# Optimization experiments

Hardware: AMD Instinct MI355X
Metric: run time of the kernel (lower is better)

## Reference

```python
import jax, jax.numpy as jnp
import numpy as np

T, S, W, D, C, K = 16, 16, 10, 512, 64, 512  # tasks, shots, ways, z_dim, n_concept, triplets/group


def setup_inputs() -> dict:
    key = jax.random.key(0)
    ks = jax.random.split(key, 12)
    sc = 0.02
    inp = {
        "input_data": jax.random.normal(ks[0], (T, S, W, D), dtype=jnp.float32),
        "triplet_idx": jax.random.randint(ks[1], (T, W, 3, K), 0, S * W, dtype=jnp.int64),
        # proj_inner: Linear(3D -> 2D), ReLU, Linear(2D -> D)
        "W1": jax.random.normal(ks[2], (3 * D, 2 * D), dtype=jnp.float32) * sc,
        "b1": jnp.zeros((2 * D,), dtype=jnp.float32),
        "W2": jax.random.normal(ks[3], (2 * D, D), dtype=jnp.float32) * sc,
        "b2": jnp.zeros((D,), dtype=jnp.float32),
        # proj_outer: Linear(D -> 2D), ReLU, Linear(2D -> D)
        "W3": jax.random.normal(ks[4], (D, 2 * D), dtype=jnp.float32) * sc,
        "b3": jnp.zeros((2 * D,), dtype=jnp.float32),
        "W4": jax.random.normal(ks[5], (2 * D, D), dtype=jnp.float32) * sc,
        "b4": jnp.zeros((D,), dtype=jnp.float32),
        # cls: Linear(D -> C)
        "Wc": jax.random.normal(ks[6], (D, C), dtype=jnp.float32) * sc,
        "bc": jnp.zeros((C,), dtype=jnp.float32),
    }
    return inp


def reference(input_data, triplet_idx, W1, b1, W2, b2, W3, b3, W4, b4, Wc, bc):
    t, s, w, d = input_data.shape
    x = input_data.reshape(t, s * w, d)                     # [T, N, D], N = shot*way
    # gather triplet embeddings: [T, W, 3, K, D]
    emb = x[jnp.arange(t)[:, None, None, None], triplet_idx]
    # permute([1,0,2]).reshape(-1, 3*dim): [T, W, K, 3*D]
    trip = jnp.swapaxes(emb, 2, 3).reshape(t, w, -1, 3 * d)
    # proj_inner MLP then sum over triplets
    h = jax.nn.relu(trip @ W1 + b1) @ W2 + b2               # [T, W, K, D]
    g = jnp.sum(h, axis=2)                                  # [T, W, D]
    # proj_outer MLP -> cls -> softmax
    o = jax.nn.relu(g @ W3 + b3) @ W4 + b4                  # [T, W, D]
    score = o @ Wc + bc                                     # [T, W, C]
    return jax.nn.softmax(score, axis=-1)
```

## Files before the change

### kernel.cpp

```cpp
#include <hip/hip_runtime.h>
#include <hip/hip_bf16.h>

#define T_  16
#define W_  10
#define D_  512
#define SW_ 160
#define N1_ 1024
#define KT_ 512

typedef __bf16 bf16x8 __attribute__((ext_vector_type(8)));
typedef _Float16 f16x8 __attribute__((ext_vector_type(8)));
typedef _Float16 h2v  __attribute__((ext_vector_type(2)));
typedef float  f32x4  __attribute__((ext_vector_type(4)));

__device__ __forceinline__ void async16(const void* g, void* l) {
  __builtin_amdgcn_global_load_lds(
      (__attribute__((address_space(1))) void*)(g),
      (__attribute__((address_space(3))) void*)(l), 16, 0, 0);
}

__device__ __forceinline__ h2v bc2(unsigned u) { return __builtin_bit_cast(h2v, u); }
__device__ __forceinline__ h2v relu2(h2v a) {
  h2v r;
  asm("v_pk_max_f16 %0, %1, 0" : "=v"(r) : "v"(a));
  return r;
}

__global__ __launch_bounds__(256) void prep_all(
    const float* __restrict__ x_in, const float* __restrict__ W1,
    const float* __restrict__ W2, const float* __restrict__ W3,
    const float* __restrict__ W4, const float* __restrict__ Wc,
    const float* __restrict__ b2, const float* __restrict__ b3,
    const float* __restrict__ b4, const float* __restrict__ bc,
    __hip_bfloat16* __restrict__ xbf, __hip_bfloat16* __restrict__ w1t,
    _Float16* __restrict__ w2b, _Float16* __restrict__ w3t,
    _Float16* __restrict__ w4b, _Float16* __restrict__ wct,
    float* __restrict__ b23, float* __restrict__ bc4)
{
  __shared__ float tile[32 * 33];
  const int b = blockIdx.x, tid = threadIdx.x;

  auto cast4h = [&](const float* src, _Float16* dst, int base) {
    int i = (base + tid) << 2;
    float4 v = *(const float4*)(src + i);
    __align__(8) _Float16 o4[4] = {(_Float16)v.x, (_Float16)v.y,
                                   (_Float16)v.z, (_Float16)v.w};
    *(uint2*)(dst + i) = *(const uint2*)o4;
  };
  auto tr32h = [&](const float* src, _Float16* dst, int R, int C, int rt, int ct) {
    int r0 = rt << 5, c0 = ct << 5;
    int c = tid & 31, rr = tid >> 5;
#pragma unroll
    for (int i = 0; i < 4; ++i) {
      int r = rr + i * 8;
      tile[r * 33 + c] = src[(size_t)(r0 + r) * C + c0 + c];
    }
    __syncthreads();
#pragma unroll
    for (int i = 0; i < 4; ++i) {
      int r = rr + i * 8;
      dst[(size_t)(c0 + r) * R + r0 + c] = (_Float16)tile[c * 33 + r];
    }
  };

  if (b < 1280) {
    int i = (b * 256 + tid) << 2;
    float4 v = *(const float4*)(x_in + i);
    __align__(8) __hip_bfloat16 o4[4];
    o4[0] = __float2bfloat16(v.x); o4[1] = __float2bfloat16(v.y);
    o4[2] = __float2bfloat16(v.z); o4[3] = __float2bfloat16(v.w);
    *(uint2*)(xbf + i) = *(const uint2*)o4;
  } else if (b < 2816) {
    int q = b - 1280;
    int r0 = (q >> 5) << 5, c0 = (q & 31) << 5;
    int c = tid & 31, rr = tid >> 5;
#pragma unroll
    for (int i = 0; i < 4; ++i) {
      int r = rr + i * 8;
      tile[r * 33 + c] = W1[(size_t)(r0 + r) * 1024 + c0 + c];
    }
    __syncthreads();
#pragma unroll
    for (int i = 0; i < 4; ++i) {
      int r = rr + i * 8;
      w1t[(size_t)(c0 + r) * 1536 + r0 + c] = __float2bfloat16(tile[c * 33 + r]);
    }
  } else if (b < 3328) {
    cast4h(W2, w2b, (b - 2816) * 256);
  } else if (b < 3840) {
    int q = b - 3328; tr32h(W3, w3t, 512, 1024, q >> 5, q & 31);
  } else if (b < 4352) {
    cast4h(W4, w4b, (b - 3840) * 256);
  } else if (b < 4384) {
    int q = b - 4352; tr32h(Wc, wct, 512, 64, q >> 1, q & 1);
  } else if (b < 4388) {
    int c = (b - 4384) * 256 + tid;
    float s = 0.f;
#pragma unroll 32
    for (int j = 0; j < 512; ++j) s += b2[j] * W3[(size_t)j * 1024 + c];
    b23[c] = 512.f * s + b3[c];
  } else {
    if (tid < 64) {
      float s = 0.f;
#pragma unroll 32
      for (int j = 0; j < 512; ++j) s += b4[j] * Wc[(size_t)j * 64 + tid];
      bc4[tid] = s + bc[tid];
    }
  }
}

__global__ __launch_bounds__(256) void pgemm_wgemm(
    const __hip_bfloat16* __restrict__ xbf,
    const __hip_bfloat16* __restrict__ w1t,
    const float* __restrict__ b1,
    char* __restrict__ pbuf,
    const _Float16* __restrict__ w3t,
    const _Float16* __restrict__ w2b,
    const _Float16* __restrict__ wct,
    const _Float16* __restrict__ w4b,
    _Float16* __restrict__ w23t,
    _Float16* __restrict__ w4ct)
{
  __shared__ __align__(16) char smem[34560];
  const int bx = blockIdx.x;
  const int tid = threadIdx.x;
  const int ln = tid & 63, wv = tid >> 6;
  const int col16 = ln & 15, quad = ln >> 4;

  if (bx >= 512) {
    const int b = bx - 512;
    const _Float16 *A, *Bt;
    _Float16* out;
    int m0, n0;
    if (b < 256) { A = w3t; Bt = w2b; out = w23t; m0 = (b >> 4) << 6; n0 = (b & 15) << 6; }
    else         { A = wct; Bt = w4b; out = w4ct; m0 = 0;             n0 = (b - 256) << 6; }
    char* Abuf = smem;
    char* Bbuf = smem + 16384;

    f32x4 acc[4];
#pragma unroll
    for (int a = 0; a < 4; ++a) acc[a] = (f32x4){0.f, 0.f, 0.f, 0.f};

#pragma unroll 1
    for (int kk = 0; kk < 512; kk += 128) {
      __syncthreads();
#pragma unroll
      for (int p = 0; p < 4; ++p) {
        int i = p * 256 + tid, r = i >> 4, q = i & 15;
        async16(A + (size_t)(m0 + r) * 512 + kk + ((q ^ (r & 7)) << 3), Abuf + (i << 4));
      }
#pragma unroll
      for (int p = 0; p < 4; ++p) {
        int i = p * 256 + tid, r = i >> 4, q = i & 15;
        async16(Bt + (size_t)(n0 + r) * 512 + kk + ((q ^ (r & 7)) << 3), Bbuf + (i << 4));
      }
      __syncthreads();

#pragma unroll
      for (int ks = 0; ks < 4; ++ks) {
        const int qq = (ks << 2) + quad;
        const int rn = (wv << 4) + col16;
        f16x8 bfm = *(const f16x8*)(Bbuf + rn * 256 + ((qq ^ (rn & 7)) << 4));
#pragma unroll
        for (int a = 0; a < 4; ++a) {
          int rm = (a << 4) + col16;
          f16x8 af = *(const f16x8*)(Abuf + rm * 256 + ((qq ^ (rm & 7)) << 4));
          acc[a] = __builtin_amdgcn_mfma_f32_16x16x32_f16(af, bfm, acc[a], 0, 0, 0);
        }
      }
    }

    const int n = n0 + (wv << 4) + col16;
#pragma unroll
    for (int a = 0; a < 4; ++a)
#pragma unroll
      for (int r = 0; r < 4; ++r) {
        size_t row = m0 + (a << 4) + (quad << 2) + r;
        out[row * 1024 + n] = (_Float16)acc[a][r];
      }
    return;
  }

  char* Abuf  = smem;
  char* Bbuf  = smem + 20480;
  char* Ptile = smem;

  const int t   = bx >> 5;
  const int nt  = bx & 31;
  const int n0  = nt << 5;

  const int wr = wv >> 1, wc = wv & 1;

  const __hip_bfloat16* xt = xbf + (size_t)t * (SW_ * D_);

  int aoff[5], lofA[5];
#pragma unroll
  for (int s = 0; s < 5; ++s) {
    int i = s * 256 + tid, r = i >> 3, q = i & 7;
    aoff[s] = r * 512 + ((q ^ (r & 7)) << 3);
    lofA[s] = i << 4;
  }
  int boff[3], lofB[3];
#pragma unroll
  for (int s = 0; s < 3; ++s) {
    int i = s * 256 + tid, r = i >> 3, q = i & 7;
    int nc = r & 31, j = r >> 5;
    boff[s] = (n0 + nc) * 1536 + j * 512 + ((q ^ (r & 7)) << 3);
    lofB[s] = i << 4;
  }

  f32x4 acc[5][3];
#pragma unroll
  for (int a = 0; a < 5; ++a)
#pragma unroll
    for (int b = 0; b < 3; ++b)
      acc[a][b] = (f32x4){0.f, 0.f, 0.f, 0.f};

#pragma unroll 1
  for (int kk = 0; kk < 512; kk += 64) {
    __syncthreads();
#pragma unroll
    for (int s = 0; s < 5; ++s) async16(xt + aoff[s] + kk, Abuf + lofA[s]);
#pragma unroll
    for (int s = 0; s < 3; ++s) async16(w1t + boff[s] + kk, Bbuf + lofB[s]);
    __syncthreads();

#pragma unroll
    for (int ks = 0; ks < 2; ++ks) {
      const int qq = (ks << 2) + quad;
      bf16x8 af[5], bfr[3];
#pragma unroll
      for (int a = 0; a < 5; ++a) {
        int rm = wr * 80 + a * 16 + col16;
        af[a] = *(const bf16x8*)(Abuf + rm * 128 + ((qq ^ (rm & 7)) << 4));
      }
#pragma unroll
      for (int b = 0; b < 3; ++b) {
        int rn = wc * 48 + b * 16 + col16;
        bfr[b] = *(const bf16x8*)(Bbuf + rn * 128 + ((qq ^ (rn & 7)) << 4));
      }
#pragma unroll
      for (int a = 0; a < 5; ++a)
#pragma unroll
        for (int b = 0; b < 3; ++b)
          acc[a][b] = __builtin_amdgcn_mfma_f32_16x16x32_bf16(af[a], bfr[b], acc[a][b], 0, 0, 0);
    }
  }

  __syncthreads();

#pragma unroll
  for (int b = 0; b < 3; ++b) {
    int c = wc * 48 + b * 16 + col16;
    int j = c >> 5, nc = c & 31;
    float bv = (j == 2) ? b1[n0 + nc] : 0.f;
#pragma unroll
    for (int a = 0; a < 5; ++a) {
      int mb = wr * 80 + a * 16 + quad * 4;
#pragma unroll
      for (int r = 0; r < 4; ++r)
        *(_Float16*)(Ptile + (j * 160 + mb + r) * 72 + nc * 2) =
            (_Float16)(acc[a][b][r] + bv);
    }
  }
  __syncthreads();

  char* gP = pbuf + (size_t)bx * 34560;
#pragma unroll
  for (int p = 0; p < 9; ++p) {
    int i = p * 256 + tid;
    if (i < 2160)
      *(uint4*)(gP + (size_t)i * 16) = *(const uint4*)(Ptile + i * 16);
  }
}

__global__ __launch_bounds__(256) void gather_kernel(
    const char* __restrict__ pbuf,
    const int* __restrict__ tidx,
    _Float16* __restrict__ Hsb)
{
  __shared__ __align__(16) char P[34560];
  __shared__ int idx[2][1536];
  __shared__ float red[2][128];
  const int tid = threadIdx.x;
  const int wp  = blockIdx.x;
  const int win = blockIdx.y;
  const int t   = blockIdx.z;
  const int ln = tid & 63, wv = tid >> 6;

  const char* ps = pbuf + (size_t)(t * 32 + win) * 34560;
#pragma unroll
  for (int p = 0; p < 9; ++p) {
    int i = p * 256 + tid;
    if (i < 2160) async16(ps + (size_t)i * 16, P + i * 16);
  }

  const int* isrc = tidx + (size_t)(t * 10 + wp * 2) * 1536;
#pragma unroll
  for (int v = 0; v < 2; ++v) {
    const int* s = isrc + v * 1536;
    int4 ra = *(const int4*)(s + (tid << 2));
    *(int4*)(&idx[v][tid << 2]) =
        make_int4(ra.x * 72, ra.y * 72, ra.z * 72, ra.w * 72);
    if (tid < 128) {
      int4 rb = *(const int4*)(s + 1024 + (tid << 2));
      *(int4*)(&idx[v][1024 + (tid << 2)]) =
          make_int4(rb.x * 72, rb.y * 72, rb.z * 72, rb.w * 72);
    }
  }
  __syncthreads();

  const int nq = tid & 7;
  const int kq = tid >> 3;
  const char* Pt0 = P + (nq << 3);
  const char* Pt1 = Pt0 + 11520;
  const char* Pt2 = Pt0 + 23040;

#pragma unroll
  for (int v = 0; v < 2; ++v) {
    const int* cid = idx[v];
    h2v acc01 = (h2v)0, acc23 = (h2v)0;
#pragma unroll
    for (int u = 0; u < 4; ++u) {
      const int kb = (kq << 4) + (u << 2);
      int4 i0 = *(const int4*)(cid + kb);
      int4 i1 = *(const int4*)(cid + 512 + kb);
      int4 i2 = *(const int4*)(cid + 1024 + kb);
#define STEP(IA, IB, IC)                                                  \
      {                                                                   \
        uint2 p0 = *(const uint2*)(Pt0 + (IA));                           \
        uint2 p1 = *(const uint2*)(Pt1 + (IB));                           \
        uint2 p2 = *(const uint2*)(Pt2 + (IC));                           \
        h2v sx = bc2(p0.x) + bc2(p1.x) + bc2(p2.x);                       \
        h2v sy = bc2(p0.y) + bc2(p1.y) + bc2(p2.y);                       \
        acc01 += relu2(sx);                                               \
        acc23 += relu2(sy);                                               \
      }
      STEP(i0.x, i1.x, i2.x)
      STEP(i0.y, i1.y, i2.y)
      STEP(i0.z, i1.z, i2.z)
      STEP(i0.w, i1.w, i2.w)
#undef STEP
    }

    f32x4 a4 = (f32x4){(float)acc01.x, (float)acc01.y,
                       (float)acc23.x, (float)acc23.y};
#pragma unroll
    for (int off = 8; off <= 32; off <<= 1) {
      a4.x += __shfl_xor(a4.x, off);
      a4.y += __shfl_xor(a4.y, off);
      a4.z += __shfl_xor(a4.z, off);
      a4.w += __shfl_xor(a4.w, off);
    }
    if ((ln >> 3) == 0)
      *(f32x4*)(&red[v][wv * 32 + (nq << 2)]) = a4;
  }
  __syncthreads();
  if (tid < 64) {
    int v = tid >> 5, c = tid & 31;
    float s = red[v][c] + red[v][32 + c] + red[v][64 + c] + red[v][96 + c];
    Hsb[(size_t)(t * 10 + wp * 2 + v) * N1_ + (win << 5) + c] = (_Float16)s;
  }
}

__global__ __launch_bounds__(256) void mid_gemm(
    const _Float16* __restrict__ A,
    const _Float16* __restrict__ Bt,
    const float* __restrict__ bias,
    _Float16* __restrict__ out)
{
  __shared__ __align__(16) char Abuf[40960];
  __shared__ __align__(16) char Bbuf[32768];
  const int tid = threadIdx.x;
  const int n0 = blockIdx.x << 6;
  const int m0 = blockIdx.y * 80;
  const int ln = tid & 63, wv = tid >> 6;
  const int col16 = ln & 15, quad = ln >> 4;

  f32x4 acc[5];
#pragma unroll
  for (int a = 0; a < 5; ++a) acc[a] = (f32x4){0.f, 0.f, 0.f, 0.f};

#pragma unroll 1
  for (int kk = 0; kk < 1024; kk += 256) {
    __syncthreads();
#pragma unroll
    for (int p = 0; p < 10; ++p) {
      int i = p * 256 + tid, r = i >> 5, q = i & 31;
      async16(A + (size_t)(m0 + r) * 1024 + kk + ((q ^ (r & 7)) << 3), Abuf + (i << 4));
    }
#pragma unroll
    for (int p = 0; p < 8; ++p) {
      int i = p * 256 + tid, r = i >> 5, q = i & 31;
      async16(Bt + (size_t)(n0 + r) * 1024 + kk + ((q ^ (r & 7)) << 3), Bbuf + (i << 4));
    }
    __syncthreads();

#pragma unroll
    for (int ks = 0; ks < 8; ++ks) {
      const int qq = (ks << 2) + quad;
      const int rn = (wv << 4) + col16;
      f16x8 bfm = *(const f16x8*)(Bbuf + rn * 512 + ((qq ^ (rn & 7)) << 4));
#pragma unroll
      for (int a = 0; a < 5; ++a) {
        int rm = (a << 4) + col16;
        f16x8 af = *(const f16x8*)(Abuf + rm * 512 + ((qq ^ (rm & 7)) << 4));
        acc[a] = __builtin_amdgcn_mfma_f32_16x16x32_f16(af, bfm, acc[a], 0, 0, 0);
      }
    }
  }

  const int n = n0 + (wv << 4) + col16;
  const float bb = bias[n];
#pragma unroll
  for (int a = 0; a < 5; ++a)
#pragma unroll
    for (int r = 0; r < 4; ++r) {
      float v = fmaxf(acc[a][r] + bb, 0.f);
      out[(size_t)(m0 + (a << 4) + (quad << 2) + r) * 1024 + n] = (_Float16)v;
    }
}

__global__ __launch_bounds__(256) void head_gemm2(
    const _Float16* __restrict__ A,
    const _Float16* __restrict__ Bt,
    const float* __restrict__ bc4,
    float* __restrict__ out)
{
  __shared__ __align__(16) char Abuf[40960];
  __shared__ __align__(16) char Bbuf[32768];
  __shared__ float sc[80 * 64];
  __shared__ float rs[80];
  const int tid = threadIdx.x;
  const int m0 = blockIdx.x * 80;
  const int ln = tid & 63, wv = tid >> 6;
  const int col16 = ln & 15, quad = ln >> 4;

  f32x4 acc[5];
#pragma unroll
  for (int a = 0; a < 5; ++a) acc[a] = (f32x4){0.f, 0.f, 0.f, 0.f};

#pragma unroll 1
  for (int kk = 0; kk < 1024; kk += 256) {
    __syncthreads();
#pragma unroll
    for (int p = 0; p < 10; ++p) {
      int i = p * 256 + tid, r = i >> 5, q = i & 31;
      async16(A + (size_t)(m0 + r) * 1024 + kk + ((q ^ (r & 7)) << 3), Abuf + (i << 4));
    }
#pragma unroll
    for (int p = 0; p < 8; ++p) {
      int i = p * 256 + tid, r = i >> 5, q = i & 31;
      async16(Bt + (size_t)r * 1024 + kk + ((q ^ (r & 7)) << 3), Bbuf + (i << 4));
    }
    __syncthreads();

#pragma unroll
    for (int ks = 0; ks < 8; ++ks) {
      const int qq = (ks << 2) + quad;
      const int rn = (wv << 4) + col16;
      f16x8 bfm = *(const f16x8*)(Bbuf + rn * 512 + ((qq ^ (rn & 7)) << 4));
#pragma unroll
      for (int a = 0; a < 5; ++a) {
        int rm = (a << 4) + col16;
        f16x8 af = *(const f16x8*)(Abuf + rm * 512 + ((qq ^ (rm & 7)) << 4));
        acc[a] = __builtin_amdgcn_mfma_f32_16x16x32_f16(af, bfm, acc[a], 0, 0, 0);
      }
    }
  }

  const int n = (wv << 4) + col16;
  const float bb = bc4[n];
#pragma unroll
  for (int a = 0; a < 5; ++a)
#pragma unroll
    for (int r = 0; r < 4; ++r)
      sc[((a << 4) + (quad << 2) + r) * 64 + n] = acc[a][r] + bb;
  __syncthreads();

  if (tid < 80) {
    float m = -1e30f;
    for (int c = 0; c < 64; ++c) m = fmaxf(m, sc[tid * 64 + c]);
    float s = 0.f;
    for (int c = 0; c < 64; ++c) {
      float e = expf(sc[tid * 64 + c] - m);
      sc[tid * 64 + c] = e;
      s += e;
    }
    rs[tid] = 1.f / s;
  }
  __syncthreads();
#pragma unroll
  for (int p = 0; p < 20; ++p) {
    int f = p * 256 + tid, r = f >> 6, c = f & 63;
    out[(size_t)(m0 + r) * 64 + c] = sc[f] * rs[r];
  }
}

extern "C" void kernel_launch(void* const* d_in, const int* in_sizes, int n_in,
                              void* d_out, int out_size, void* d_ws, size_t ws_size,
                              hipStream_t stream) {
  const float* x_in = (const float*)d_in[0];
  const int*   tidx = (const int*)d_in[1];
  const float* W1 = (const float*)d_in[2];
  const float* b1 = (const float*)d_in[3];
  const float* W2 = (const float*)d_in[4];
  const float* b2 = (const float*)d_in[5];
  const float* W3 = (const float*)d_in[6];
  const float* b3 = (const float*)d_in[7];
  const float* W4 = (const float*)d_in[8];
  const float* b4 = (const float*)d_in[9];
  const float* Wc = (const float*)d_in[10];
  const float* bc = (const float*)d_in[11];
  float* out = (float*)d_out;
  (void)in_sizes; (void)n_in; (void)out_size; (void)ws_size;

  char* ws = (char*)d_ws;
  __hip_bfloat16* xbf  = (__hip_bfloat16*)(ws + 0);
  __hip_bfloat16* w1t  = (__hip_bfloat16*)(ws + 2621440);
  _Float16*       w2b  = (_Float16*)      (ws + 5767168);
  _Float16*       w3t  = (_Float16*)      (ws + 6815744);
  _Float16*       w4b  = (_Float16*)      (ws + 7864320);
  _Float16*       wct  = (_Float16*)      (ws + 8912896);
  float*          b23  = (float*)         (ws + 8978432);
  float*          bc4  = (float*)         (ws + 8982528);
  _Float16*       Hsb  = (_Float16*)      (ws + 8982784);
  _Float16*       w23t = (_Float16*)      (ws + 9310464);
  _Float16*       w4ct = (_Float16*)      (ws + 11407616);
  char*           pbuf = ws + 11538688;
  _Float16*       ub   = (_Float16*)      (ws + 11538688);

  prep_all<<<4389, 256, 0, stream>>>(x_in, W1, W2, W3, W4, Wc, b2, b3, b4, bc,
                                     xbf, w1t, w2b, w3t, w4b, wct, b23, bc4);

  pgemm_wgemm<<<784, 256, 0, stream>>>(xbf, w1t, b1, pbuf,
                                       w3t, w2b, wct, w4b, w23t, w4ct);

  gather_kernel<<<dim3(5, 32, 16), 256, 0, stream>>>(pbuf, tidx, Hsb);

  mid_gemm<<<dim3(16, 2), 256, 0, stream>>>(Hsb, w23t, b23, ub);

  head_gemm2<<<2, 256, 0, stream>>>(ub, w4ct, bc4, out);
}
```

Measured before the change: 160.7 us.

## Fuse triplet gather into projection GEMM and fold head GEMM into mid GEMM

The gather/sum stage now runs inside the projection GEMM block. Each block keeps its projected tile in shared memory and loops over the five way-pairs, double-buffering the triplet indices, so the intermediate buffer is never written to and re-read from global memory. The head GEMM is fused into the mid GEMM epilogue as per-column-block partial scores, and a small softmax kernel sums the partials. The projection K-step also widens from 64 to 128, which enlarges shared memory to 64KB and may reduce occupancy.

```diff
diff --git a/kernel.cpp b/kernel.cpp
--- a/kernel.cpp
+++ b/kernel.cpp
@@ -109,11 +109,12 @@
   }
 }
 
-__global__ __launch_bounds__(256) void pgemm_wgemm(
+__global__ __launch_bounds__(256) void group_wgemm(
     const __hip_bfloat16* __restrict__ xbf,
     const __hip_bfloat16* __restrict__ w1t,
+    const int* __restrict__ tidx,
     const float* __restrict__ b1,
-    char* __restrict__ pbuf,
+    _Float16* __restrict__ Hsb,
     const _Float16* __restrict__ w3t,
     const _Float16* __restrict__ w2b,
     const _Float16* __restrict__ wct,
@@ -121,7 +122,7 @@
     _Float16* __restrict__ w23t,
     _Float16* __restrict__ w4ct)
 {
-  __shared__ __align__(16) char smem[34560];
+  __shared__ __align__(16) char smem[65536];
   const int bx = blockIdx.x;
   const int tid = threadIdx.x;
   const int ln = tid & 63, wv = tid >> 6;
@@ -182,8 +183,10 @@
   }
 
   char* Abuf  = smem;
-  char* Bbuf  = smem + 20480;
+  char* Bbuf  = smem + 40960;
   char* Ptile = smem;
+  int*  ibuf  = (int*)(smem + 34560);
+  float* red  = (float*)(smem + 59136);
 
   const int t   = bx >> 5;
   const int nt  = bx & 31;
@@ -193,17 +196,17 @@
 
   const __hip_bfloat16* xt = xbf + (size_t)t * (SW_ * D_);
 
-  int aoff[5], lofA[5];
-#pragma unroll
-  for (int s = 0; s < 5; ++s) {
-    int i = s * 256 + tid, r = i >> 3, q = i & 7;
+  int aoff[10], lofA[10];
+#pragma unroll
+  for (int s = 0; s < 10; ++s) {
+    int i = s * 256 + tid, r = i >> 4, q = i & 15;
     aoff[s] = r * 512 + ((q ^ (r & 7)) << 3);
     lofA[s] = i << 4;
   }
-  int boff[3], lofB[3];
-#pragma unroll
-  for (int s = 0; s < 3; ++s) {
-    int i = s * 256 + tid, r = i >> 3, q = i & 7;
+  int boff[6], lofB[6];
+#pragma unroll
+  for (int s = 0; s < 6; ++s) {
+    int i = s * 256 + tid, r = i >> 4, q = i & 15;
     int nc = r & 31, j = r >> 5;
     boff[s] = (n0 + nc) * 1536 + j * 512 + ((q ^ (r & 7)) << 3);
     lofB[s] = i << 4;
@@ -217,27 +220,27 @@
       acc[a][b] = (f32x4){0.f, 0.f, 0.f, 0.f};
 
 #pragma unroll 1
-  for (int kk = 0; kk < 512; kk += 64) {
-    __syncthreads();
-#pragma unroll
-    for (int s = 0; s < 5; ++s) async16(xt + aoff[s] + kk, Abuf + lofA[s]);
-#pragma unroll
-    for (int s = 0; s < 3; ++s) async16(w1t + boff[s] + kk, Bbuf + lofB[s]);
-    __syncthreads();
-
-#pragma unroll
-    for (int ks = 0; ks < 2; ++ks) {
+  for (int kk = 0; kk < 512; kk += 128) {
+    __syncthreads();
+#pragma unroll
+    for (int s = 0; s < 10; ++s) async16(xt + aoff[s] + kk, Abuf + lofA[s]);
+#pragma unroll
+    for (int s = 0; s < 6; ++s) async16(w1t + boff[s] + kk, Bbuf + lofB[s]);
+    __syncthreads();
+
+#pragma unroll
+    for (int ks = 0; ks < 4; ++ks) {
       const int qq = (ks << 2) + quad;
       bf16x8 af[5], bfr[3];
 #pragma unroll
       for (int a = 0; a < 5; ++a) {
         int rm = wr * 80 + a * 16 + col16;
-        af[a] = *(const bf16x8*)(Abuf + rm * 128 + ((qq ^ (rm & 7)) << 4));
+        af[a] = *(const bf16x8*)(Abuf + rm * 256 + ((qq ^ (rm & 7)) << 4));
       }
 #pragma unroll
       for (int b = 0; b < 3; ++b) {
         int rn = wc * 48 + b * 16 + col16;
-        bfr[b] = *(const bf16x8*)(Bbuf + rn * 128 + ((qq ^ (rn & 7)) << 4));
+        bfr[b] = *(const bf16x8*)(Bbuf + rn * 256 + ((qq ^ (rn & 7)) << 4));
       }
 #pragma unroll
       for (int a = 0; a < 5; ++a)
@@ -263,120 +266,127 @@
             (_Float16)(acc[a][b][r] + bv);
     }
   }
-  __syncthreads();
-
-  char* gP = pbuf + (size_t)bx * 34560;
-#pragma unroll
-  for (int p = 0; p < 9; ++p) {
-    int i = p * 256 + tid;
-    if (i < 2160)
-      *(uint4*)(gP + (size_t)i * 16) = *(const uint4*)(Ptile + i * 16);
-  }
-}
-
-__global__ __launch_bounds__(256) void gather_kernel(
-    const char* __restrict__ pbuf,
-    const int* __restrict__ tidx,
-    _Float16* __restrict__ Hsb)
-{
-  __shared__ __align__(16) char P[34560];
-  __shared__ int idx[2][1536];
-  __shared__ float red[2][128];
-  const int tid = threadIdx.x;
-  const int wp  = blockIdx.x;
-  const int win = blockIdx.y;
-  const int t   = blockIdx.z;
-  const int ln = tid & 63, wv = tid >> 6;
-
-  const char* ps = pbuf + (size_t)(t * 32 + win) * 34560;
-#pragma unroll
-  for (int p = 0; p < 9; ++p) {
-    int i = p * 256 + tid;
-    if (i < 2160) async16(ps + (size_t)i * 16, P + i * 16);
-  }
-
-  const int* isrc = tidx + (size_t)(t * 10 + wp * 2) * 1536;
-#pragma unroll
-  for (int v = 0; v < 2; ++v) {
-    const int* s = isrc + v * 1536;
-    int4 ra = *(const int4*)(s + (tid << 2));
-    *(int4*)(&idx[v][tid << 2]) =
-        make_int4(ra.x * 72, ra.y * 72, ra.z * 72, ra.w * 72);
-    if (tid < 128) {
-      int4 rb = *(const int4*)(s + 1024 + (tid << 2));
-      *(int4*)(&idx[v][1024 + (tid << 2)]) =
-          make_int4(rb.x * 72, rb.y * 72, rb.z * 72, rb.w * 72);
-    }
-  }
-  __syncthreads();
 
   const int nq = tid & 7;
   const int kq = tid >> 3;
-  const char* Pt0 = P + (nq << 3);
+  const char* Pt0 = Ptile + (nq << 3);
   const char* Pt1 = Pt0 + 11520;
   const char* Pt2 = Pt0 + 23040;
 
+  const int* tsrc = tidx + (size_t)t * 10 * 1536;
+  int4 ra[2], rb[2];
+  auto sst2 = [&](int* dstbase) {
+#pragma unroll
+    for (int v = 0; v < 2; ++v) {
+      int* dst = dstbase + v * 1536;
+      *(int4*)(dst + (tid << 2)) =
+          make_int4(ra[v].x * 72, ra[v].y * 72, ra[v].z * 72, ra[v].w * 72);
+      if (tid < 128)
+        *(int4*)(dst + 1024 + (tid << 2)) =
+            make_int4(rb[v].x * 72, rb[v].y * 72, rb[v].z * 72, rb[v].w * 72);
+    }
+  };
+
 #pragma unroll
   for (int v = 0; v < 2; ++v) {
-    const int* cid = idx[v];
-    h2v acc01 = (h2v)0, acc23 = (h2v)0;
-#pragma unroll
-    for (int u = 0; u < 4; ++u) {
-      const int kb = (kq << 4) + (u << 2);
-      int4 i0 = *(const int4*)(cid + kb);
-      int4 i1 = *(const int4*)(cid + 512 + kb);
-      int4 i2 = *(const int4*)(cid + 1024 + kb);
+    const int* s0 = tsrc + v * 1536;
+    ra[v] = *(const int4*)(s0 + (tid << 2));
+    if (tid < 128) rb[v] = *(const int4*)(s0 + 1024 + (tid << 2));
+  }
+  sst2(ibuf);
+  int cur = 0;
+
+#pragma unroll 1
+  for (int wp = 0; wp < 5; ++wp) {
+    __syncthreads();
+    if (wp < 4) {
+#pragma unroll
+      for (int v = 0; v < 2; ++v) {
+        const int* s2 = tsrc + (wp * 2 + 2 + v) * 1536;
+        ra[v] = *(const int4*)(s2 + (tid << 2));
+        if (tid < 128) rb[v] = *(const int4*)(s2 + 1024 + (tid << 2));
+      }
+    }
+
+    const int* cb = ibuf + cur * 3072;
+    f32x4 a4[2];
+#pragma unroll
+    for (int v = 0; v < 2; ++v) {
+      const int* cid = cb + v * 1536;
+      h2v acc01 = (h2v)0, acc23 = (h2v)0;
+#pragma unroll
+      for (int u = 0; u < 4; ++u) {
+        const int kb = (kq << 4) + (u << 2);
+        int4 i0 = *(const int4*)(cid + kb);
+        int4 i1 = *(const int4*)(cid + 512 + kb);
+        int4 i2 = *(const int4*)(cid + 1024 + kb);
 #define STEP(IA, IB, IC)                                                  \
-      {                                                                   \
-        uint2 p0 = *(const uint2*)(Pt0 + (IA));                           \
-        uint2 p1 = *(const uint2*)(Pt1 + (IB));                           \
-        uint2 p2 = *(const uint2*)(Pt2 + (IC));                           \
-        h2v sx = bc2(p0.x) + bc2(p1.x) + bc2(p2.x);                       \
-        h2v sy = bc2(p0.y) + bc2(p1.y) + bc2(p2.y);                       \
-        acc01 += relu2(sx);                                               \
-        acc23 += relu2(sy);                                               \
-      }
-      STEP(i0.x, i1.x, i2.x)
-      STEP(i0.y, i1.y, i2.y)
-      STEP(i0.z, i1.z, i2.z)
-      STEP(i0.w, i1.w, i2.w)
+        {                                                                 \
+          uint2 p0 = *(const uint2*)(Pt0 + (IA));                         \
+          uint2 p1 = *(const uint2*)(Pt1 + (IB));                         \
+          uint2 p2 = *(const uint2*)(Pt2 + (IC));                         \
+          h2v sx = bc2(p0.x) + bc2(p1.x) + bc2(p2.x);                     \
+          h2v sy = bc2(p0.y) + bc2(p1.y) + bc2(p2.y);                     \
+          acc01 += relu2(sx);                                             \
+          acc23 += relu2(sy);                                             \
+        }
+        STEP(i0.x, i1.x, i2.x)
+        STEP(i0.y, i1.y, i2.y)
+        STEP(i0.z, i1.z, i2.z)
+        STEP(i0.w, i1.w, i2.w)
 #undef STEP
-    }
-
-    f32x4 a4 = (f32x4){(float)acc01.x, (float)acc01.y,
-                       (float)acc23.x, (float)acc23.y};
-#pragma unroll
-    for (int off = 8; off <= 32; off <<= 1) {
-      a4.x += __shfl_xor(a4.x, off);
-      a4.y += __shfl_xor(a4.y, off);
-      a4.z += __shfl_xor(a4.z, off);
-      a4.w += __shfl_xor(a4.w, off);
-    }
-    if ((ln >> 3) == 0)
-      *(f32x4*)(&red[v][wv * 32 + (nq << 2)]) = a4;
-  }
-  __syncthreads();
-  if (tid < 64) {
-    int v = tid >> 5, c = tid & 31;
-    float s = red[v][c] + red[v][32 + c] + red[v][64 + c] + red[v][96 + c];
-    Hsb[(size_t)(t * 10 + wp * 2 + v) * N1_ + (win << 5) + c] = (_Float16)s;
-  }
-}
-
-__global__ __launch_bounds__(256) void mid_gemm(
+      }
+      a4[v] = (f32x4){(float)acc01.x, (float)acc01.y,
+                      (float)acc23.x, (float)acc23.y};
+    }
+
+    if (wp < 4) sst2(ibuf + (cur ^ 1) * 3072);
+
+#pragma unroll
+    for (int v = 0; v < 2; ++v) {
+#pragma unroll
+      for (int off = 8; off <= 32; off <<= 1) {
+        a4[v].x += __shfl_xor(a4[v].x, off);
+        a4[v].y += __shfl_xor(a4[v].y, off);
+        a4[v].z += __shfl_xor(a4[v].z, off);
+        a4[v].w += __shfl_xor(a4[v].w, off);
+      }
+      if ((ln >> 3) == 0)
+        *(f32x4*)(red + v * 128 + wv * 32 + (nq << 2)) = a4[v];
+    }
+    __syncthreads();
+    if (tid < 64) {
+      int v = tid >> 5, c = tid & 31;
+      const float* rv = red + v * 128;
+      float s = rv[c] + rv[32 + c] + rv[64 + c] + rv[96 + c];
+      Hsb[(size_t)(t * 10 + wp * 2 + v) * N1_ + n0 + c] = (_Float16)s;
+    }
+    cur ^= 1;
+  }
+}
+
+__global__ __launch_bounds__(256) void mid_head(
     const _Float16* __restrict__ A,
     const _Float16* __restrict__ Bt,
+    const _Float16* __restrict__ W4c,
     const float* __restrict__ bias,
-    _Float16* __restrict__ out)
+    float* __restrict__ psc)
 {
   __shared__ __align__(16) char Abuf[40960];
   __shared__ __align__(16) char Bbuf[32768];
+  __shared__ __align__(16) char Hbuf[8192];
   const int tid = threadIdx.x;
   const int n0 = blockIdx.x << 6;
   const int m0 = blockIdx.y * 80;
   const int ln = tid & 63, wv = tid >> 6;
   const int col16 = ln & 15, quad = ln >> 4;
 
+#pragma unroll
+  for (int p = 0; p < 2; ++p) {
+    int i = p * 256 + tid, r = i >> 3, q = i & 7;
+    async16(W4c + (size_t)r * 1024 + n0 + ((q ^ (r & 7)) << 3), Hbuf + (i << 4));
+  }
+
   f32x4 acc[5];
 #pragma unroll
   for (int a = 0; a < 5; ++a) acc[a] = (f32x4){0.f, 0.f, 0.f, 0.f};
@@ -410,72 +420,65 @@
     }
   }
 
-  const int n = n0 + (wv << 4) + col16;
-  const float bb = bias[n];
+  const float bb = bias[n0 + (wv << 4) + col16];
+  __syncthreads();
+  char* U = Abuf;
+  const int cl = (wv << 4) + col16;
 #pragma unroll
   for (int a = 0; a < 5; ++a)
 #pragma unroll
     for (int r = 0; r < 4; ++r) {
       float v = fmaxf(acc[a][r] + bb, 0.f);
-      out[(size_t)(m0 + (a << 4) + (quad << 2) + r) * 1024 + n] = (_Float16)v;
-    }
-}
-
-__global__ __launch_bounds__(256) void head_gemm2(
-    const _Float16* __restrict__ A,
-    const _Float16* __restrict__ Bt,
+      int m = (a << 4) + (quad << 2) + r;
+      *(_Float16*)(U + m * 128 + (((cl >> 3) ^ (m & 7)) << 4) + ((cl & 7) << 1)) =
+          (_Float16)v;
+    }
+  __syncthreads();
+
+  f32x4 acc2[5];
+#pragma unroll
+  for (int a = 0; a < 5; ++a) acc2[a] = (f32x4){0.f, 0.f, 0.f, 0.f};
+#pragma unroll
+  for (int ks = 0; ks < 2; ++ks) {
+    const int qq = (ks << 2) + quad;
+    const int rn = (wv << 4) + col16;
+    f16x8 bfm = *(const f16x8*)(Hbuf + rn * 128 + ((qq ^ (rn & 7)) << 4));
+#pragma unroll
+    for (int a = 0; a < 5; ++a) {
+      int rm = (a << 4) + col16;
+      f16x8 af = *(const f16x8*)(U + rm * 128 + ((qq ^ (rm & 7)) << 4));
+      acc2[a] = __builtin_amdgcn_mfma_f32_16x16x32_f16(af, bfm, acc2[a], 0, 0, 0);
+    }
+  }
+  float* po = psc + ((size_t)blockIdx.x * 160 + m0) * 64;
+#pragma unroll
+  for (int a = 0; a < 5; ++a)
+#pragma unroll
+    for (int r = 0; r < 4; ++r)
+      po[((a << 4) + (quad << 2) + r) * 64 + (wv << 4) + col16] = acc2[a][r];
+}
+
+__global__ __launch_bounds__(256) void softmax2(
+    const float* __restrict__ psc,
     const float* __restrict__ bc4,
     float* __restrict__ out)
 {
-  __shared__ __align__(16) char Abuf[40960];
-  __shared__ __align__(16) char Bbuf[32768];
   __shared__ float sc[80 * 64];
   __shared__ float rs[80];
   const int tid = threadIdx.x;
   const int m0 = blockIdx.x * 80;
-  const int ln = tid & 63, wv = tid >> 6;
-  const int col16 = ln & 15, quad = ln >> 4;
-
-  f32x4 acc[5];
-#pragma unroll
-  for (int a = 0; a < 5; ++a) acc[a] = (f32x4){0.f, 0.f, 0.f, 0.f};
-
-#pragma unroll 1
-  for (int kk = 0; kk < 1024; kk += 256) {
-    __syncthreads();
-#pragma unroll
-    for (int p = 0; p < 10; ++p) {
-      int i = p * 256 + tid, r = i >> 5, q = i & 31;
-      async16(A + (size_t)(m0 + r) * 1024 + kk + ((q ^ (r & 7)) << 3), Abuf + (i << 4));
-    }
-#pragma unroll
-    for (int p = 0; p < 8; ++p) {
-      int i = p * 256 + tid, r = i >> 5, q = i & 31;
-      async16(Bt + (size_t)r * 1024 + kk + ((q ^ (r & 7)) << 3), Bbuf + (i << 4));
-    }
-    __syncthreads();
-
-#pragma unroll
-    for (int ks = 0; ks < 8; ++ks) {
-      const int qq = (ks << 2) + quad;
-      const int rn = (wv << 4) + col16;
-      f16x8 bfm = *(const f16x8*)(Bbuf + rn * 512 + ((qq ^ (rn & 7)) << 4));
-#pragma unroll
-      for (int a = 0; a < 5; ++a) {
-        int rm = (a << 4) + col16;
-        f16x8 af = *(const f16x8*)(Abuf + rm * 512 + ((qq ^ (rm & 7)) << 4));
-        acc[a] = __builtin_amdgcn_mfma_f32_16x16x32_f16(af, bfm, acc[a], 0, 0, 0);
-      }
-    }
-  }
-
-  const int n = (wv << 4) + col16;
-  const float bb = bc4[n];
-#pragma unroll
-  for (int a = 0; a < 5; ++a)
-#pragma unroll
-    for (int r = 0; r < 4; ++r)
-      sc[((a << 4) + (quad << 2) + r) * 64 + n] = acc[a][r] + bb;
+
+#pragma unroll
+  for (int p = 0; p < 5; ++p) {
+    int f = p * 256 + tid;
+    int r = f >> 4, cq = f & 15;
+    f32x4 s = (f32x4){0.f, 0.f, 0.f, 0.f};
+#pragma unroll
+    for (int j = 0; j < 16; ++j)
+      s += *(const f32x4*)(psc + ((size_t)(j * 160) + m0 + r) * 64 + (cq << 2));
+    s += *(const f32x4*)(bc4 + (cq << 2));
+    *(f32x4*)(sc + r * 64 + (cq << 2)) = s;
+  }
   __syncthreads();
 
   if (tid < 80) {
@@ -527,18 +530,15 @@
   _Float16*       Hsb  = (_Float16*)      (ws + 8982784);
   _Float16*       w23t = (_Float16*)      (ws + 9310464);
   _Float16*       w4ct = (_Float16*)      (ws + 11407616);
-  char*           pbuf = ws + 11538688;
-  _Float16*       ub   = (_Float16*)      (ws + 11538688);
+  float*          psc  = (float*)         (ws + 11538688);
 
   prep_all<<<4389, 256, 0, stream>>>(x_in, W1, W2, W3, W4, Wc, b2, b3, b4, bc,
                                      xbf, w1t, w2b, w3t, w4b, wct, b23, bc4);
 
-  pgemm_wgemm<<<784, 256, 0, stream>>>(xbf, w1t, b1, pbuf,
+  group_wgemm<<<784, 256, 0, stream>>>(xbf, w1t, tidx, b1, Hsb,
                                        w3t, w2b, wct, w4b, w23t, w4ct);
 
-  gather_kernel<<<dim3(5, 32, 16), 256, 0, stream>>>(pbuf, tidx, Hsb);
-
-  mid_gemm<<<dim3(16, 2), 256, 0, stream>>>(Hsb, w23t, b23, ub);
-
-  head_gemm2<<<2, 256, 0, stream>>>(ub, w4ct, bc4, out);
-}
+  mid_head<<<dim3(16, 2), 256, 0, stream>>>(Hsb, w23t, w4ct, b23, psc);
+
+  softmax2<<<2, 256, 0, stream>>>(psc, bc4, out);
+}
```

Result: faster. 146.7 us (-8.7%).
